# Kernel optimization log

Hardware: AMD Instinct MI355X
Metric: run time of the kernel (lower is better)

The kernel has to match this reference:

```python
import math
import jax, jax.numpy as jnp
import numpy as np

COULOMB = 14.399645478425668  # eV*Angstrom / e^2


def setup_inputs() -> dict:
    key = jax.random.key(0)
    k0, k1, k2, k3, k4 = jax.random.split(key, 5)
    B, n, F, S = 128, 512, 64, 4  # molecules, atoms/molecule, feat dim, n species
    N = B * n
    node_features = jax.random.normal(k0, (N, F), dtype=jnp.float32)
    pos = jax.random.normal(k1, (N, 3), dtype=jnp.float32) * 5.0  # spread atoms out
    atom_type = jax.random.randint(k2, (N,), 0, S)
    total_charge = jnp.zeros((B, 1), dtype=jnp.float32)
    chi_weight = jax.random.normal(k3, (F, 1), dtype=jnp.float32) / np.float32(np.sqrt(F))
    hardness_param = jnp.ones((S,), dtype=jnp.float32)
    sigma = 0.3 + 0.5 * jax.random.uniform(k4, (S,), dtype=jnp.float32)  # covalent radii
    return dict(node_features=node_features, pos=pos, atom_type=atom_type,
                total_charge=total_charge, chi_weight=chi_weight,
                hardness_param=hardness_param, sigma=sigma, n_per_mol=n)


def reference(node_features, pos, atom_type, total_charge, chi_weight,
              hardness_param, sigma, n_per_mol):
    n = n_per_mol
    N, F = node_features.shape
    B = N // n

    feats = node_features.reshape(B, n, F)
    pos_b = pos.reshape(B, n, 3)
    sp = atom_type.reshape(B, n)

    chi = (feats @ chi_weight)[..., 0]                      # [B, n] electronegativity
    hard = jnp.square(hardness_param)[sp]                   # [B, n]
    sig = sigma[sp]                                         # [B, n]

    # pairwise distances within each molecule (diag masked for safe divide)
    diff = pos_b[:, :, None, :] - pos_b[:, None, :, :]      # [B, n, n, 3]
    d2 = jnp.sum(diff * diff, axis=-1)
    eye = jnp.eye(n, dtype=pos.dtype)
    d = jnp.sqrt(jnp.where(eye, 1.0, d2))                   # [B, n, n]

    gamma = jnp.sqrt(sig[:, :, None] ** 2 + sig[:, None, :] ** 2)
    off = COULOMB * jax.lax.erf(d / (math.sqrt(2.0) * gamma)) / d
    diag = hard + COULOMB / (math.sqrt(math.pi) * sig)      # [B, n]
    coeffs = off * (1.0 - eye) + eye * diag[:, :, None]     # [B, n, n]

    # augmented Qeq system with charge-conservation Lagrange multiplier
    A = jnp.ones((B, n + 1, n + 1), dtype=coeffs.dtype)
    A = A.at[:, :n, :n].set(coeffs)
    A = A.at[:, n, n].set(0.0)
    rhs = jnp.concatenate([-chi, total_charge], axis=1)     # [B, n+1]
    sol = jnp.linalg.solve(A, rhs[..., None])[..., 0]
    q = sol[:, :n]                                          # [B, n] charges

    # E = sum_{i<j} C_ij q_i q_j + sum_i (chi_i q_i + 0.5 diag_i q_i^2)
    #   = 0.5 q^T C q + chi . q   (C includes diagonal)
    e_qeq = 0.5 * jnp.einsum('bi,bij,bj->b', q, coeffs, q) + jnp.sum(chi * q, axis=1)
    return e_qeq[:, None], q.reshape(N, 1)
```

## Files before the change

kernel.cpp:

```cpp
#include <hip/hip_runtime.h>
#include <math.h>

#define NA 512
#define NN (NA*NA)
#define COULOMB 14.399645478425668f
#define SQRT_PI 1.7724538509055160273f

typedef float v2f __attribute__((ext_vector_type(2)));

__device__ __forceinline__ float rl(float x, int lane) {
    return __int_as_float(__builtin_amdgcn_readlane(__float_as_int(x), lane));
}

__device__ __forceinline__ float pair_val(float dx, float dy, float dz,
                                          float s2i, float s2k) {
    float d2 = dx*dx + dy*dy + dz*dz;
    float rinv = rsqrtf(d2);
    return COULOMB * erff(d2 * rinv * rsqrtf(2.f * (s2i + s2k))) * rinv;
}

__global__ void k_pre(const float* __restrict__ feats, const float* __restrict__ w,
                      const int* __restrict__ type, const float* __restrict__ hard,
                      const float* __restrict__ sigma,
                      float* __restrict__ chi, float* __restrict__ diag,
                      float* __restrict__ sigA,
                      float* __restrict__ r1, float* __restrict__ r2, int N) {
    __shared__ float wl[64];
    int tid = threadIdx.x;
    if (tid < 64) wl[tid] = w[tid];
    __syncthreads();
    int i = blockIdx.x * 256 + tid;
    if (i >= N) return;
    const float4* fp = (const float4*)(feats + (size_t)i * 64);
    float acc = 0.f;
#pragma unroll
    for (int q = 0; q < 16; q++) {
        float4 v = fp[q];
        acc += v.x * wl[4*q] + v.y * wl[4*q+1] + v.z * wl[4*q+2] + v.w * wl[4*q+3];
    }
    chi[i] = acc;
    r1[i] = acc;
    r2[i] = 1.0f;
    int t = type[i];
    float s = sigma[t];
    float h = hard[t];
    sigA[i] = s;
    diag[i] = h * h + COULOMB / (SQRT_PI * s);
}

__global__ void __launch_bounds__(256, 1) k_panel(const float* __restrict__ pos,
                                                  const float* __restrict__ sigA,
                                                  const float* __restrict__ diagA,
                                                  float* __restrict__ C,
                                                  float* __restrict__ r1,
                                                  float* __restrict__ r2, const int j) {
    const int q = blockIdx.x;
    const int b = blockIdx.y;
    float* __restrict__ Cb = C + (size_t)b * NN;
    const int jb = j * 64;
    const int m = NA - jb - 64;
    const int tid = threadIdx.x;
    __shared__ float D[64 * 65];
    __shared__ float DT[64 * 64];
    __shared__ float invd[64];
    __shared__ float y1s[64], y2s[64];
    __shared__ float px[NA], py[NA], pz[NA], s2s[NA];

    if (j == 0) {
#pragma unroll
        for (int e = 0; e < 2; e++) {
            int i = e * 256 + tid;
            px[i] = pos[((size_t)b * NA + i) * 3 + 0];
            py[i] = pos[((size_t)b * NA + i) * 3 + 1];
            pz[i] = pos[((size_t)b * NA + i) * 3 + 2];
            float s = sigA[b * NA + i];
            s2s[i] = s * s;
        }
        __syncthreads();
    }

#pragma unroll
    for (int e = 0; e < 16; e++) {
        int f = e * 256 + tid;
        int rr = f >> 6, cc = f & 63;
        float v;
        if (j == 0) {
            if (rr == cc) v = diagA[b * NA + rr];
            else v = pair_val(px[rr]-px[cc], py[rr]-py[cc], pz[rr]-pz[cc], s2s[rr], s2s[cc]);
        } else {
            v = Cb[(size_t)(jb + rr) * NA + jb + cc];
        }
        D[rr * 65 + cc] = v;
    }

    const int h = m >> 1;
    const int r0 = q ? h : 0;
    const int nr = q ? (m - h) : h;
    const int r = tid - 32;
    const bool hasrow = (r >= 0 && r < nr);
    const int grow = jb + 64 + r0 + r;
    float rv[64];
    if (hasrow) {
        if (j == 0) {
#pragma unroll
            for (int k = 0; k < 64; k++)
                rv[k] = pair_val(px[grow]-px[k], py[grow]-py[k], pz[grow]-pz[k],
                                 s2s[grow], s2s[k]);
        } else {
            const float4* rp = (const float4*)(Cb + (size_t)grow * NA + jb);
#pragma unroll
            for (int qq = 0; qq < 16; qq++) {
                float4 v = rp[qq];
                rv[4*qq] = v.x; rv[4*qq+1] = v.y; rv[4*qq+2] = v.z; rv[4*qq+3] = v.w;
            }
        }
    }
    __syncthreads();

    if (tid < 64) {
        const int t = tid;
        float cl[64];
#pragma unroll
        for (int i = 0; i < 64; i++) cl[i] = (i >= t) ? D[i * 65 + t] : D[t * 65 + i];
#pragma unroll
        for (int k = 0; k < 64; k++) {
            float pivot = rl(cl[k], k);
            float invp = 1.0f / pivot;
            float factor = (t > k) ? (cl[k] * invp) : 0.0f;
#pragma unroll
            for (int i = k + 1; i < 64; i++) {
                float bc = rl(cl[i], k);
                cl[i] -= bc * factor;
            }
        }
        float rs = 1.0f / sqrtf(cl[t]);
        invd[t] = rs;
#pragma unroll
        for (int i = 0; i < 64; i++)
            if (i >= t) D[i * 65 + t] = cl[i] * rs;

        float v1 = r1[(size_t)b * NA + jb + t];
        float v2 = r2[(size_t)b * NA + jb + t];
#pragma unroll
        for (int k = 0; k < 64; k++) {
            float rsk = rl(rs, k);
            float y1k = rl(v1, k) * rsk;
            float y2k = rl(v2, k) * rsk;
            if (t == k) {
                y1s[t] = y1k; y2s[t] = y2k;
                if (q == 0) {
                    r1[(size_t)b * NA + jb + t] = y1k;
                    r2[(size_t)b * NA + jb + t] = y2k;
                }
            }
            float lv = (t > k) ? D[t * 65 + k] : 0.f;
            v1 -= lv * y1k;
            v2 -= lv * y2k;
        }
    }
    __syncthreads();

#pragma unroll
    for (int e = 0; e < 16; e++) {
        int f = e * 256 + tid;
        int row = f >> 6, cc = f & 63;
        float v = D[row * 65 + cc];
        DT[row * 64 + cc] = (cc < row) ? v : 0.f;
        if (q == 0 && cc <= row) Cb[(size_t)(jb + row) * NA + jb + cc] = v;
    }
    __syncthreads();

    if (hasrow) {
#pragma unroll
        for (int k = 0; k < 64; k++) {
            float acc = rv[k];
            const float4* Lr = (const float4*)(DT + k * 64);
            const int k4 = k >> 2;
#pragma unroll
            for (int t4 = 0; t4 < k4; t4++) {
                float4 Lv = Lr[t4];
                acc -= Lv.x * rv[4*t4] + Lv.y * rv[4*t4+1] + Lv.z * rv[4*t4+2] + Lv.w * rv[4*t4+3];
            }
#pragma unroll
            for (int tt = k4 * 4; tt < k; tt++) acc -= DT[k * 64 + tt] * rv[tt];
            rv[k] = acc * invd[k];
        }
        float4* rp = (float4*)(Cb + (size_t)grow * NA + jb);
#pragma unroll
        for (int qq = 0; qq < 16; qq++)
            rp[qq] = make_float4(rv[4*qq], rv[4*qq+1], rv[4*qq+2], rv[4*qq+3]);

        float a1 = 0.f, a2 = 0.f;
#pragma unroll
        for (int k = 0; k < 64; k++) {
            a1 = fmaf(rv[k], y1s[k], a1);
            a2 = fmaf(rv[k], y2s[k], a2);
        }
        r1[(size_t)b * NA + grow] -= a1;
        r2[(size_t)b * NA + grow] -= a2;
    }
}

template<bool GEN>
__global__ void __launch_bounds__(256, 2) k_trail(float* __restrict__ C,
                                                  const float* __restrict__ pos,
                                                  const float* __restrict__ sigA,
                                                  const float* __restrict__ diagA,
                                                  const int j) {
    const int b = blockIdx.y;
    float* __restrict__ Cb = C + (size_t)b * NN;
    const int jb = j * 64;
    const int m = NA - jb - 64;
    int t = blockIdx.x;
    int RI = 0;
    while (t >= RI + 1) { t -= RI + 1; RI++; }
    const int RJ = t;
    const int RB = RI * 128, CB = RJ * 128;
    const int vr = min(128, m - RB);
    const int vc = min(128, m - CB);
    const int tid = threadIdx.x;
    const int rg = tid >> 4, cg = tid & 15;

    __shared__ float As[128 * 66];
    __shared__ float Bs[128 * 66];

    v2f ac2[8][8];

    if (GEN) {
        __shared__ float pAx[128], pAy[128], pAz[128], sA[128], dA[128];
        __shared__ float pBx[128], pBy[128], pBz[128], sB[128];
        if (tid < 128) {
            if (RB + tid < m) {
                int ga = b * NA + jb + 64 + RB + tid;
                pAx[tid] = pos[(size_t)ga * 3 + 0];
                pAy[tid] = pos[(size_t)ga * 3 + 1];
                pAz[tid] = pos[(size_t)ga * 3 + 2];
                float s = sigA[ga]; sA[tid] = s * s;
                dA[tid] = diagA[ga];
            }
        } else {
            int u = tid - 128;
            if (CB + u < m) {
                int gb = b * NA + jb + 64 + CB + u;
                pBx[u] = pos[(size_t)gb * 3 + 0];
                pBy[u] = pos[(size_t)gb * 3 + 1];
                pBz[u] = pos[(size_t)gb * 3 + 2];
                float s = sigA[gb]; sB[u] = s * s;
            }
        }
        __syncthreads();
#pragma unroll
        for (int rr = 0; rr < 8; rr++) {
            int row = rg * 8 + rr;
#pragma unroll
            for (int cc = 0; cc < 8; cc++) {
                int col = cg + 16 * cc;
                float iv;
                if (RB + row == CB + col)
                    iv = dA[row];
                else
                    iv = pair_val(pAx[row]-pBx[col], pAy[row]-pBy[col],
                                  pAz[row]-pBz[col], sA[row], sB[col]);
                ac2[rr][cc].x = iv;
                ac2[rr][cc].y = 0.f;
            }
        }
        __syncthreads();
    } else {
        const int GRB = jb + 64 + RB, GCB = jb + 64 + CB;
#pragma unroll
        for (int rr = 0; rr < 8; rr++) {
            int row = rg * 8 + rr;
#pragma unroll
            for (int cc = 0; cc < 8; cc++) {
                int col = cg + 16 * cc;
                ac2[rr][cc].x = (row < vr && col < vc)
                    ? Cb[(size_t)(GRB + row) * NA + GCB + col] : 0.f;
                ac2[rr][cc].y = 0.f;
            }
        }
    }

    const float* Pan = Cb + (size_t)(jb + 64) * NA + jb;
#pragma unroll
    for (int e = 0; e < 8; e++) {
        int f = e * 256 + tid;
        int row = f >> 4, s = f & 15;
        float4 v = make_float4(0.f, 0.f, 0.f, 0.f);
        if (row < vr) v = *(const float4*)(Pan + (size_t)(RB + row) * NA + s * 4);
        As[row * 66 + s * 4 + 0] = v.x;
        As[row * 66 + s * 4 + 1] = v.y;
        As[row * 66 + s * 4 + 2] = v.z;
        As[row * 66 + s * 4 + 3] = v.w;
        float4 u = make_float4(0.f, 0.f, 0.f, 0.f);
        if (row < vc) u = *(const float4*)(Pan + (size_t)(CB + row) * NA + s * 4);
        Bs[row * 66 + s * 4 + 0] = u.x;
        Bs[row * 66 + s * 4 + 1] = u.y;
        Bs[row * 66 + s * 4 + 2] = u.z;
        Bs[row * 66 + s * 4 + 3] = u.w;
    }
    __syncthreads();

#pragma unroll 2
    for (int k = 0; k < 64; k += 2) {
        v2f ai2[8], bj2[8];
#pragma unroll
        for (int rr = 0; rr < 8; rr++)
            ai2[rr] = *(const v2f*)&As[(rg * 8 + rr) * 66 + k];
#pragma unroll
        for (int cc = 0; cc < 8; cc++)
            bj2[cc] = *(const v2f*)&Bs[(cg + 16 * cc) * 66 + k];
#pragma unroll
        for (int rr = 0; rr < 8; rr++)
#pragma unroll
            for (int cc = 0; cc < 8; cc++) {
                ac2[rr][cc].x = fmaf(-ai2[rr].x, bj2[cc].x, ac2[rr][cc].x);
                ac2[rr][cc].y = fmaf(-ai2[rr].y, bj2[cc].y, ac2[rr][cc].y);
            }
    }

    const int GRB = jb + 64 + RB, GCB = jb + 64 + CB;
#pragma unroll
    for (int rr = 0; rr < 8; rr++) {
        int row = rg * 8 + rr;
        if (row < vr) {
#pragma unroll
            for (int cc = 0; cc < 8; cc++) {
                int col = cg + 16 * cc;
                if (col < vc)
                    Cb[(size_t)(GRB + row) * NA + GCB + col] = ac2[rr][cc].x + ac2[rr][cc].y;
            }
        }
    }
}

__global__ void __launch_bounds__(512, 1) k_back(const float* __restrict__ C,
                                                 float* __restrict__ r1g,
                                                 float* __restrict__ r2g) {
    const int b = blockIdx.x;
    const int rhs = blockIdx.y;
    const float* Cb = C + (size_t)b * NN;
    const int tid = threadIdx.x;
    __shared__ float D[64 * 65];
    __shared__ float r[NA];
    __shared__ float pb[4][NA];

    float* rg = rhs ? r2g : r1g;
    r[tid] = rg[(size_t)b * NA + tid];

    const int ii = tid & 127;
    const int gg = tid >> 7;
    for (int j = 7; j >= 0; j--) {
        const int jb = j * 64;
        __syncthreads();
#pragma unroll
        for (int e = 0; e < 8; e++) {
            int f = e * 512 + tid;
            int row = f >> 6, cc = f & 63;
            D[row * 65 + cc] = Cb[(size_t)(jb + row) * NA + jb + cc];
        }
        __syncthreads();
        if (tid < 64) {
            float val = r[jb + tid];
            float idg = 1.0f / D[tid * 65 + tid];
#pragma unroll
            for (int k = 63; k >= 0; k--) {
                float xk = rl(val, k) * rl(idg, k);
                if (tid == k) r[jb + k] = xk;
                float lv = (tid < k) ? D[k * 65 + tid] : 0.f;
                val -= lv * xk;
            }
        }
        __syncthreads();
        if (jb > 0) {
            const int nf4 = jb >> 2;
            float4 s1 = make_float4(0.f, 0.f, 0.f, 0.f);
            if (ii < nf4) {
#pragma unroll
                for (int gq = 0; gq < 16; gq++) {
                    int g = jb + gg * 16 + gq;
                    float x1 = r[g];
                    float4 Lv = *(const float4*)(Cb + (size_t)g * NA + ii * 4);
                    s1.x += Lv.x * x1; s1.y += Lv.y * x1; s1.z += Lv.z * x1; s1.w += Lv.w * x1;
                }
            }
            *(float4*)(&pb[gg][ii * 4]) = s1;
            __syncthreads();
            if (tid < jb)
                r[tid] -= pb[0][tid] + pb[1][tid] + pb[2][tid] + pb[3][tid];
        }
    }
    __syncthreads();

    rg[(size_t)b * NA + tid] = r[tid];
}

__global__ void __launch_bounds__(512, 1) k_final(const float* __restrict__ x1,
                                                  const float* __restrict__ x2,
                                                  const float* __restrict__ chiA,
                                                  const float* __restrict__ Qtot,
                                                  float* __restrict__ out, int B) {
    const int b = blockIdx.x;
    const int tid = threadIdx.x;
    __shared__ float red[16];
    __shared__ float muS;

    float v1 = x1[(size_t)b * NA + tid];
    float v2 = x2[(size_t)b * NA + tid];

    float s1p = v1, s2p = v2;
#pragma unroll
    for (int off = 1; off < 64; off <<= 1) {
        s1p += __shfl_xor(s1p, off);
        s2p += __shfl_xor(s2p, off);
    }
    if ((tid & 63) == 0) { red[tid >> 6] = s1p; red[8 + (tid >> 6)] = s2p; }
    __syncthreads();
    if (tid == 0) {
        float s1 = 0.f, s2 = 0.f;
#pragma unroll
        for (int wv = 0; wv < 8; wv++) { s1 += red[wv]; s2 += red[8 + wv]; }
        muS = -(Qtot[b] + s1) / s2;
    }
    __syncthreads();
    float mu = muS;
    float qv = -v1 - mu * v2;
    out[B + (size_t)b * NA + tid] = qv;

    float eacc = chiA[b * NA + tid] * qv;
#pragma unroll
    for (int off = 1; off < 64; off <<= 1) eacc += __shfl_xor(eacc, off);
    __syncthreads();
    if ((tid & 63) == 0) red[tid >> 6] = eacc;
    __syncthreads();
    if (tid == 0) {
        float e = 0.f;
#pragma unroll
        for (int wv = 0; wv < 8; wv++) e += red[wv];
        out[b] = 0.5f * e - 0.5f * mu * Qtot[b];
    }
}

extern "C" void kernel_launch(void* const* d_in, const int* in_sizes, int n_in,
                              void* d_out, int out_size, void* d_ws, size_t ws_size,
                              hipStream_t stream) {
    const int B = in_sizes[3];
    const int N = in_sizes[2];
    const float* feats = (const float*)d_in[0];
    const float* pos   = (const float*)d_in[1];
    const int*   type  = (const int*)d_in[2];
    const float* Qt    = (const float*)d_in[3];
    const float* w     = (const float*)d_in[4];
    const float* hard  = (const float*)d_in[5];
    const float* sig   = (const float*)d_in[6];
    float* out = (float*)d_out;
    float* ws  = (float*)d_ws;

    float* C    = ws;
    float* chi  = ws + (size_t)B * NN;
    float* diag = chi + N;
    float* sigA = diag + N;
    float* r1   = sigA + N;
    float* r2   = r1 + N;

    k_pre<<<(N + 255) / 256, 256, 0, stream>>>(feats, w, type, hard, sig,
                                               chi, diag, sigA, r1, r2, N);

    static const int tilesJ[7] = {10, 6, 6, 3, 3, 1, 1};
    for (int j = 0; j < 8; j++) {
        k_panel<<<dim3(2, B), 256, 0, stream>>>(pos, sigA, diag, C, r1, r2, j);
        if (j < 7) {
            if (j == 0)
                k_trail<true><<<dim3(tilesJ[j], B), 256, 0, stream>>>(C, pos, sigA, diag, j);
            else
                k_trail<false><<<dim3(tilesJ[j], B), 256, 0, stream>>>(C, pos, sigA, diag, j);
        }
    }
    k_back<<<dim3(B, 2), 512, 0, stream>>>(C, r1, r2);
    k_final<<<B, 512, 0, stream>>>(r1, r2, chi, Qt, out, B);
}
```

Baseline: 726.6 us.

## Fuse last three Cholesky panel/trailing steps into one shared-memory tail kernel

Result: no change. 725.5 us (median of 2 runs) (-0.2%).

```diff
diff --git a/kernel.cpp b/kernel.cpp
--- a/kernel.cpp
+++ b/kernel.cpp
@@ -5,6 +5,10 @@
 #define NN (NA*NA)
 #define COULOMB 14.399645478425668f
 #define SQRT_PI 1.7724538509055160273f
+
+#define TB 320
+#define TS 192
+#define TSTR 193
 
 typedef float v2f __attribute__((ext_vector_type(2)));
 
@@ -334,6 +338,167 @@
     }
 }
 
+__global__ void __launch_bounds__(256, 1) k_tail(float* __restrict__ C,
+                                                 float* __restrict__ r1,
+                                                 float* __restrict__ r2) {
+    const int b = blockIdx.x;
+    float* __restrict__ Cb = C + (size_t)b * NN;
+    const int tid = threadIdx.x;
+    __shared__ float T[TS * TSTR];
+    __shared__ float invd[64], y1s[64], y2s[64];
+
+    for (int f = tid; f < TS * TS; f += 256) {
+        int row = f / TS, c = f - row * TS;
+        T[row * TSTR + c] = Cb[(size_t)(TB + row) * NA + TB + c];
+    }
+    __syncthreads();
+
+#pragma unroll 1
+    for (int p = 0; p < 3; p++) {
+        const int pb = p * 64;
+        const int msub = TS - pb - 64;
+
+        if (tid < 64) {
+            const int t = tid;
+            float cl[64];
+#pragma unroll
+            for (int i = 0; i < 64; i++)
+                cl[i] = (i >= t) ? T[(pb + i) * TSTR + pb + t]
+                                 : T[(pb + t) * TSTR + pb + i];
+#pragma unroll
+            for (int k = 0; k < 64; k++) {
+                float pivot = rl(cl[k], k);
+                float invp = 1.0f / pivot;
+                float factor = (t > k) ? (cl[k] * invp) : 0.0f;
+#pragma unroll
+                for (int i = k + 1; i < 64; i++) {
+                    float bc = rl(cl[i], k);
+                    cl[i] -= bc * factor;
+                }
+            }
+            float rs = 1.0f / sqrtf(cl[t]);
+            invd[t] = rs;
+#pragma unroll
+            for (int i = 0; i < 64; i++) {
+                float lv = cl[i] * rs;
+                if (i >= t) T[(pb + i) * TSTR + pb + t] = lv;
+                if (i > t)  T[(pb + t) * TSTR + pb + i] = lv;
+            }
+            float v1 = r1[(size_t)b * NA + TB + pb + t];
+            float v2 = r2[(size_t)b * NA + TB + pb + t];
+#pragma unroll
+            for (int k = 0; k < 64; k++) {
+                float rsk = rl(rs, k);
+                float y1k = rl(v1, k) * rsk;
+                float y2k = rl(v2, k) * rsk;
+                if (t == k) {
+                    y1s[t] = y1k; y2s[t] = y2k;
+                    r1[(size_t)b * NA + TB + pb + t] = y1k;
+                    r2[(size_t)b * NA + TB + pb + t] = y2k;
+                }
+                float lv = (t > k) ? T[(pb + t) * TSTR + pb + k] : 0.f;
+                v1 -= lv * y1k;
+                v2 -= lv * y2k;
+            }
+        }
+        __syncthreads();
+
+        if (msub > 0) {
+            if (tid < msub) {
+                const int row_l = pb + 64 + tid;
+                float rv[64];
+#pragma unroll
+                for (int k = 0; k < 64; k++) rv[k] = T[row_l * TSTR + pb + k];
+#pragma unroll
+                for (int k = 0; k < 64; k++) {
+                    float yk = rv[k] * invd[k];
+                    rv[k] = yk;
+                    const float* LTrow = &T[(pb + k) * TSTR + pb];
+#pragma unroll
+                    for (int i = k + 1; i < 64; i++)
+                        rv[i] -= LTrow[i] * yk;
+                }
+#pragma unroll
+                for (int k = 0; k < 64; k++) T[row_l * TSTR + pb + k] = rv[k];
+                float a1 = 0.f, a2 = 0.f;
+#pragma unroll
+                for (int k = 0; k < 64; k++) {
+                    a1 = fmaf(rv[k], y1s[k], a1);
+                    a2 = fmaf(rv[k], y2s[k], a2);
+                }
+                r1[(size_t)b * NA + TB + row_l] -= a1;
+                r2[(size_t)b * NA + TB + row_l] -= a2;
+            }
+            __syncthreads();
+
+            const int rbase = pb + 64;
+            if (p == 0) {
+                const int rg = tid >> 4, cg = tid & 15;
+                float acc[8][8];
+#pragma unroll
+                for (int rr = 0; rr < 8; rr++)
+#pragma unroll
+                    for (int cc = 0; cc < 8; cc++)
+                        acc[rr][cc] = T[(rbase + rg * 8 + rr) * TSTR + rbase + cg * 8 + cc];
+#pragma unroll 4
+                for (int k = 0; k < 64; k++) {
+                    float ai[8], bj[8];
+#pragma unroll
+                    for (int rr = 0; rr < 8; rr++)
+                        ai[rr] = T[(rbase + rg * 8 + rr) * TSTR + pb + k];
+#pragma unroll
+                    for (int cc = 0; cc < 8; cc++)
+                        bj[cc] = T[(rbase + cg * 8 + cc) * TSTR + pb + k];
+#pragma unroll
+                    for (int rr = 0; rr < 8; rr++)
+#pragma unroll
+                        for (int cc = 0; cc < 8; cc++)
+                            acc[rr][cc] = fmaf(-ai[rr], bj[cc], acc[rr][cc]);
+                }
+#pragma unroll
+                for (int rr = 0; rr < 8; rr++)
+#pragma unroll
+                    for (int cc = 0; cc < 8; cc++)
+                        T[(rbase + rg * 8 + rr) * TSTR + rbase + cg * 8 + cc] = acc[rr][cc];
+            } else {
+                const int rg = tid >> 4, cg = tid & 15;
+                float acc[4][4];
+#pragma unroll
+                for (int rr = 0; rr < 4; rr++)
+#pragma unroll
+                    for (int cc = 0; cc < 4; cc++)
+                        acc[rr][cc] = T[(rbase + rg * 4 + rr) * TSTR + rbase + cg * 4 + cc];
+#pragma unroll 4
+                for (int k = 0; k < 64; k++) {
+                    float ai[4], bj[4];
+#pragma unroll
+                    for (int rr = 0; rr < 4; rr++)
+                        ai[rr] = T[(rbase + rg * 4 + rr) * TSTR + pb + k];
+#pragma unroll
+                    for (int cc = 0; cc < 4; cc++)
+                        bj[cc] = T[(rbase + cg * 4 + cc) * TSTR + pb + k];
+#pragma unroll
+                    for (int rr = 0; rr < 4; rr++)
+#pragma unroll
+                        for (int cc = 0; cc < 4; cc++)
+                            acc[rr][cc] = fmaf(-ai[rr], bj[cc], acc[rr][cc]);
+                }
+#pragma unroll
+                for (int rr = 0; rr < 4; rr++)
+#pragma unroll
+                    for (int cc = 0; cc < 4; cc++)
+                        T[(rbase + rg * 4 + rr) * TSTR + rbase + cg * 4 + cc] = acc[rr][cc];
+            }
+        }
+        __syncthreads();
+    }
+
+    for (int f = tid; f < TS * TS; f += 256) {
+        int row = f / TS, c = f - row * TS;
+        Cb[(size_t)(TB + row) * NA + TB + c] = T[row * TSTR + c];
+    }
+}
+
 __global__ void __launch_bounds__(512, 1) k_back(const float* __restrict__ C,
                                                  float* __restrict__ r1g,
                                                  float* __restrict__ r2g) {
@@ -466,16 +631,15 @@
     k_pre<<<(N + 255) / 256, 256, 0, stream>>>(feats, w, type, hard, sig,
                                                chi, diag, sigA, r1, r2, N);
 
-    static const int tilesJ[7] = {10, 6, 6, 3, 3, 1, 1};
-    for (int j = 0; j < 8; j++) {
+    static const int tilesJ[5] = {10, 6, 6, 3, 3};
+    for (int j = 0; j < 5; j++) {
         k_panel<<<dim3(2, B), 256, 0, stream>>>(pos, sigA, diag, C, r1, r2, j);
-        if (j < 7) {
-            if (j == 0)
-                k_trail<true><<<dim3(tilesJ[j], B), 256, 0, stream>>>(C, pos, sigA, diag, j);
-            else
-                k_trail<false><<<dim3(tilesJ[j], B), 256, 0, stream>>>(C, pos, sigA, diag, j);
-        }
-    }
+        if (j == 0)
+            k_trail<true><<<dim3(tilesJ[j], B), 256, 0, stream>>>(C, pos, sigA, diag, j);
+        else
+            k_trail<false><<<dim3(tilesJ[j], B), 256, 0, stream>>>(C, pos, sigA, diag, j);
+    }
+    k_tail<<<B, 256, 0, stream>>>(C, r1, r2);
     k_back<<<dim3(B, 2), 512, 0, stream>>>(C, r1, r2);
     k_final<<<B, 512, 0, stream>>>(r1, r2, chi, Qt, out, B);
 }
```
